# Optimization experiments

Measured on AMD Instinct MI355X. Metric: run time of the kernel, lower is better.

Reference implementation:

```python
import jax, jax.numpy as jnp
import numpy as np

G = 4          # number of product sub-quantizers
K = 1024       # codebook_size per sub-quantizer
D = 256        # full feature dim
d = D // G     # sub-dim per quantizer
DECAY = 0.99
EPS = 1e-5


def setup_inputs() -> dict:
    key = jax.random.key(0)
    k1, k2, k3, k4 = jax.random.split(key, 4)
    x = jax.random.normal(k1, (8, 4096, D), jnp.float32)
    embed = jax.random.normal(k2, (G, K, d), jnp.float32)
    embed_avg = jax.random.normal(k3, (G, K, d), jnp.float32)
    cluster_size = jax.random.uniform(k4, (G, K), jnp.float32)
    return dict(x=x, embed=embed, embed_avg=embed_avg, cluster_size=cluster_size)


def reference(x, embed, embed_avg, cluster_size):
    B, S, _ = x.shape
    N = B * S
    xg = x.reshape(N, G, d)                       # [N, G, d] tokens split into sub-vectors
    x2 = jnp.sum(xg * xg, axis=-1, keepdims=True)  # [N, G, 1]
    e2 = jnp.sum(embed * embed, axis=-1)           # [G, K]
    dots = jnp.einsum('ngd,gkd->ngk', xg, embed)   # [N, G, K]
    dist = -(x2 - 2.0 * dots + e2[None, :, :])     # [N, G, K]
    # sample_codebook_temp = 0 -> gumbel_sample degenerates to argmax
    ind = jnp.argmax(dist, axis=-1)                # [N, G]
    # quantized vectors: gather from each group's codebook
    zq = embed[jnp.arange(G)[None, :], ind]        # [N, G, d]
    # --- EMA buffer updates (training path) via scatter/segment-sum ---
    flat_ids = (ind + jnp.arange(G)[None, :] * K).reshape(-1)  # [N*G]
    counts = jax.ops.segment_sum(
        jnp.ones_like(flat_ids, dtype=jnp.float32), flat_ids,
        num_segments=G * K).reshape(G, K)
    embed_sum = jax.ops.segment_sum(
        xg.reshape(N * G, d), flat_ids,
        num_segments=G * K).reshape(G, K, d)
    new_cluster_size = DECAY * cluster_size + (1.0 - DECAY) * counts
    new_embed_avg = DECAY * embed_avg + (1.0 - DECAY) * embed_sum
    # laplace smoothing then renormalize codebook
    tot = jnp.sum(new_cluster_size, axis=-1, keepdims=True)       # [G, 1]
    smoothed = (new_cluster_size + EPS) / (tot + K * EPS) * tot   # [G, K]
    new_embed = new_embed_avg / smoothed[..., None]               # [G, K, d]
    return (zq.reshape(B, S, D),
            ind.reshape(B, S, G).astype(jnp.int32),
            new_embed, new_cluster_size, new_embed_avg)
```

## Files before the change

### kernel.cpp

```cpp
#include <hip/hip_runtime.h>
#include <cstdint>

#define GQ 4
#define KQ 1024
#define DQ 256
#define dq 64
#define NQ 32768
#define DECAYF 0.99f
#define EPSF 1e-5f

#define OFF_ZQ    0
#define OFF_IND   8388608
#define OFF_EMB   8519680
#define OFF_CS    8781824
#define OFF_AVG   8785920

#define WS_IND   0
#define WS_E2    524288
#define WS_EH    540672
#define WS_EL    1064960
#define WS_CTR   1589264
#define WS_LIST  1589280
#define CAP      16384
#define WS_E2D   1720352
#define WS_TOT   1753120
#define WS_PART  1753344
#define WS_PCNT  5947648

#define MARGIN 0.01f
#define FPS 65536.0f

#define MBLK 128

typedef __attribute__((ext_vector_type(8))) short bf16x8;
typedef __attribute__((ext_vector_type(4))) float f32x4;

__device__ __forceinline__ void split8_2x(float4 u, float4 v, bf16x8& h, bf16x8& l) {
    float f[8] = {u.x, u.y, u.z, u.w, v.x, v.y, v.z, v.w};
#pragma unroll
    for (int j = 0; j < 8; ++j) {
        float s = f[j] * 2.0f;
        uint32_t b = __float_as_uint(s);
        uint32_t hb = b & 0xffff0000u;
        float r = s - __uint_as_float(hb);
        uint32_t rb = __float_as_uint(r);
        h[j] = (short)(hb >> 16);
        l[j] = (short)((rb + 0x7fffu + ((rb >> 16) & 1u)) >> 16);
    }
}

__global__ void k_prep(const float* __restrict__ embed, const float* __restrict__ cs,
                       float* __restrict__ e2, double* __restrict__ e2d,
                       ushort* __restrict__ eh, ushort* __restrict__ el,
                       float* __restrict__ tot, int* __restrict__ ctr) {
    __shared__ double red[256];
    int t = blockIdx.x * 256 + threadIdx.x;
    int row = t >> 3;
    int f = t & 7;
    int c = f >> 2, l4 = f & 3;
    int g = row >> 10, k = row & 1023;
    int ch = k >> 6, co = k & 63;

    const float4* p = reinterpret_cast<const float4*>(embed + (size_t)row * dq + f * 8);
    float4 u = p[0], v = p[1];
    float fv[8] = {u.x, u.y, u.z, u.w, v.x, v.y, v.z, v.w};
    bf16x8 h, l;
    double s = 0.0;
#pragma unroll
    for (int jj = 0; jj < 8; ++jj) {
        float x = fv[jj];
        s = fma((double)x, (double)x, s);
        uint32_t b = __float_as_uint(x);
        uint32_t hb = (b + 0x7fffu + ((b >> 16) & 1u)) & 0xffff0000u;
        float r = x - __uint_as_float(hb);
        uint32_t rb = __float_as_uint(r);
        h[jj] = (short)(hb >> 16);
        l[jj] = (short)((rb + 0x7fffu + ((rb >> 16) & 1u)) >> 16);
    }
    size_t addr = (size_t)g * 65536 + (size_t)ch * 4096 + (size_t)(c * 4 + l4) * 512 + co * 8;
    *reinterpret_cast<bf16x8*>(eh + addr) = h;
    *reinterpret_cast<bf16x8*>(el + addr) = l;
    s += __shfl_xor(s, 1, 64);
    s += __shfl_xor(s, 2, 64);
    s += __shfl_xor(s, 4, 64);
    if (f == 0) { e2[row] = (float)s; e2d[row] = s; }

    if (blockIdx.x < 4) {
        int gg = blockIdx.x;
        const float4* c4 = reinterpret_cast<const float4*>(cs + gg * KQ);
        float4 cv = c4[threadIdx.x];
        red[threadIdx.x] = (double)cv.x + (double)cv.y + (double)cv.z + (double)cv.w;
        __syncthreads();
        for (int off = 128; off > 0; off >>= 1) {
            if (threadIdx.x < off) red[threadIdx.x] += red[threadIdx.x + off];
            __syncthreads();
        }
        if (threadIdx.x == 0) {
            tot[gg] = (float)((double)DECAYF * red[0] + (1.0 - (double)DECAYF) * (double)NQ);
            if (gg == 0) *ctr = 0;
        }
    }
}

__launch_bounds__(256)
__global__ void k_scores_mfma(const float* __restrict__ x,
                              const ushort* __restrict__ eh,
                              const ushort* __restrict__ el,
                              const float* __restrict__ e2,
                              const float* __restrict__ embed,
                              int* __restrict__ ind_t,
                              float* __restrict__ zq,
                              float* __restrict__ ind_out,
                              int* __restrict__ ctr, int2* __restrict__ list) {
    int g = blockIdx.y;
    int n0 = blockIdx.x * MBLK;
    int tid = threadIdx.x;
    int wid = tid >> 6;
    int lane = tid & 63;
    int l15 = lane & 15, l4 = lane >> 4;

    __shared__ ushort lds[2][8192];

    bf16x8 ah[2][2], al[2][2];
#pragma unroll
    for (int m = 0; m < 2; ++m)
#pragma unroll
        for (int c = 0; c < 2; ++c) {
            const float4* p = reinterpret_cast<const float4*>(
                x + (size_t)(n0 + wid * 32 + m * 16 + l15) * DQ + g * dq + c * 32 + l4 * 8);
            split8_2x(p[0], p[1], ah[m][c], al[m][c]);
        }

    const ushort* ehg = eh + (size_t)g * 65536;
    const ushort* elg = el + (size_t)g * 65536;
    const float*  e2g = e2 + (size_t)g * KQ;

    float m1[2][4], m2[2][4];
    int   k1[2][4];
#pragma unroll
    for (int m = 0; m < 2; ++m)
#pragma unroll
        for (int r = 0; r < 4; ++r) { m1[m][r] = -3.4e38f; m2[m][r] = -3.4e38f; k1[m][r] = 0; }

    int wu = wid * 512;
#define STAGE(b, ch)                                                               \
    do {                                                                           \
        const ushort* s0_ = ehg + (ch) * 4096 + tid * 8;                           \
        const ushort* s1_ = elg + (ch) * 4096 + tid * 8;                           \
        __builtin_amdgcn_global_load_lds(s0_,        &lds[b][wu],        16, 0, 0);\
        __builtin_amdgcn_global_load_lds(s0_ + 2048, &lds[b][2048 + wu], 16, 0, 0);\
        __builtin_amdgcn_global_load_lds(s1_,        &lds[b][4096 + wu], 16, 0, 0);\
        __builtin_amdgcn_global_load_lds(s1_ + 2048, &lds[b][6144 + wu], 16, 0, 0);\
    } while (0)

    float e2cur[4];
#pragma unroll
    for (int n = 0; n < 4; ++n) e2cur[n] = e2g[n * 16 + l15];

    STAGE(0, 0);
    int cur = 0;

#pragma unroll 1
    for (int ch = 0; ch < 16; ++ch) {
        int cb = ch * 64;
        __syncthreads();
        if (ch < 15) STAGE(cur ^ 1, ch + 1);

        float e2nxt[4];
        if (ch < 15) {
#pragma unroll
            for (int n = 0; n < 4; ++n) e2nxt[n] = e2g[cb + 64 + n * 16 + l15];
        }

        f32x4 acc[2][4];
#pragma unroll
        for (int m = 0; m < 2; ++m)
#pragma unroll
            for (int n = 0; n < 4; ++n)
                acc[m][n] = (f32x4){-e2cur[n], -e2cur[n], -e2cur[n], -e2cur[n]};

#pragma unroll
        for (int c = 0; c < 2; ++c) {
            bf16x8 bh[4], bl[4];
            int base = (c * 4 + l4) * 512 + l15 * 8;
#pragma unroll
            for (int n = 0; n < 4; ++n) {
                bh[n] = *reinterpret_cast<const bf16x8*>(&lds[cur][base + n * 128]);
                bl[n] = *reinterpret_cast<const bf16x8*>(&lds[cur][4096 + base + n * 128]);
            }
#pragma unroll
            for (int m = 0; m < 2; ++m)
#pragma unroll
                for (int n = 0; n < 4; ++n) {
                    acc[m][n] = __builtin_amdgcn_mfma_f32_16x16x32_bf16(ah[m][c], bh[n], acc[m][n], 0, 0, 0);
                    acc[m][n] = __builtin_amdgcn_mfma_f32_16x16x32_bf16(ah[m][c], bl[n], acc[m][n], 0, 0, 0);
                    acc[m][n] = __builtin_amdgcn_mfma_f32_16x16x32_bf16(al[m][c], bh[n], acc[m][n], 0, 0, 0);
                }
        }

#pragma unroll
        for (int n = 0; n < 4; ++n) {
            int col = cb + n * 16 + l15;
#pragma unroll
            for (int m = 0; m < 2; ++m)
#pragma unroll
                for (int r = 0; r < 4; ++r) {
                    float s = acc[m][n][r];
                    bool gt = s > m1[m][r];
                    m2[m][r] = __builtin_amdgcn_fmed3f(s, m1[m][r], m2[m][r]);
                    k1[m][r] = gt ? col : k1[m][r];
                    m1[m][r] = fmaxf(m1[m][r], s);
                }
        }
#pragma unroll
        for (int n = 0; n < 4; ++n) e2cur[n] = e2nxt[n];
        cur ^= 1;
    }
#undef STAGE

    int* ckk = reinterpret_cast<int*>(&lds[0][0]);

#pragma unroll
    for (int m = 0; m < 2; ++m)
#pragma unroll
        for (int r = 0; r < 4; ++r) {
            float a1 = m1[m][r], a2 = m2[m][r];
            int ak = k1[m][r];
#pragma unroll
            for (int d = 1; d < 16; d <<= 1) {
                float o1 = __shfl_xor(a1, d, 64);
                float o2 = __shfl_xor(a2, d, 64);
                int   ok = __shfl_xor(ak, d, 64);
                bool sw = (o1 > a1) || (o1 == a1 && ok < ak);
                float big = sw ? o1 : a1;
                int bigk = sw ? ok : ak;
                float small = sw ? a1 : o1;
                a2 = fmaxf(fmaxf(a2, o2), small);
                a1 = big; ak = bigk;
            }
            if (l15 == 0) {
                int rloc = m * 16 + l4 * 4 + r;
                int row = n0 + wid * 32 + rloc;
                ckk[wid * 32 + rloc] = ak;
                ind_t[(size_t)g * NQ + row] = ak;
                if (a1 - a2 < MARGIN) {
                    int idx = atomicAdd(ctr, 1);
                    if (idx < CAP) list[idx] = make_int2(row, g);
                }
            }
        }
    __syncthreads();

    if (lane < 32) {
        int row = n0 + wid * 32 + lane;
        ind_out[(size_t)row * GQ + g] = (float)ckk[wid * 32 + lane];
    }
#pragma unroll 4
    for (int rr = 0; rr < 32; ++rr) {
        int k = ckk[wid * 32 + rr];
        float v = embed[((size_t)(g * KQ + k)) * dq + lane];
        zq[(size_t)(n0 + wid * 32 + rr) * DQ + g * dq + lane] = v;
    }
}

__launch_bounds__(256)
__global__ void k_recheck(const float* __restrict__ x, const float* __restrict__ embed,
                          const double* __restrict__ e2d,
                          const int* __restrict__ ctr, const int2* __restrict__ list,
                          int* __restrict__ ind_t, float* __restrict__ zq,
                          float* __restrict__ ind_out) {
    __shared__ double sv[256];
    __shared__ int si[256];
    int nitems = *ctr;
    if (nitems > CAP) nitems = CAP;
    for (int it = blockIdx.x; it < nitems; it += gridDim.x) {
        int2 q = list[it];
        int n = q.x, g = q.y;
        const float4* xr4 = reinterpret_cast<const float4*>(x + (size_t)n * DQ + g * dq);
        float4 xr[16];
#pragma unroll
        for (int j = 0; j < 16; ++j) xr[j] = xr4[j];
        double best = -1e300;
        int bk = KQ;
        for (int k = threadIdx.x; k < KQ; k += 256) {
            const float4* er = reinterpret_cast<const float4*>(embed + ((size_t)g * KQ + k) * dq);
            double dot = 0.0;
#pragma unroll
            for (int j = 0; j < 16; ++j) {
                float4 e4 = er[j];
                dot = fma((double)xr[j].x, (double)e4.x, dot);
                dot = fma((double)xr[j].y, (double)e4.y, dot);
                dot = fma((double)xr[j].z, (double)e4.z, dot);
                dot = fma((double)xr[j].w, (double)e4.w, dot);
            }
            double s = 2.0 * dot - e2d[g * KQ + k];
            if (s > best || (s == best && k < bk)) { best = s; bk = k; }
        }
        sv[threadIdx.x] = best; si[threadIdx.x] = bk;
        __syncthreads();
        for (int off = 128; off > 0; off >>= 1) {
            if (threadIdx.x < off) {
                double ov = sv[threadIdx.x + off]; int oi = si[threadIdx.x + off];
                if (ov > sv[threadIdx.x] || (ov == sv[threadIdx.x] && oi < si[threadIdx.x])) {
                    sv[threadIdx.x] = ov; si[threadIdx.x] = oi;
                }
            }
            __syncthreads();
        }
        int kbest = si[0];
        if (threadIdx.x == 0) {
            ind_t[(size_t)g * NQ + n] = kbest;
            ind_out[(size_t)n * GQ + g] = (float)kbest;
        }
        if (threadIdx.x < dq)
            zq[(size_t)n * DQ + g * dq + threadIdx.x] =
                embed[((size_t)g * KQ + kbest) * dq + threadIdx.x];
        __syncthreads();
    }
}

#define SBINS 8
__launch_bounds__(256)
__global__ void k_segsum4(const float* __restrict__ x, const int* __restrict__ ind_t,
                          int* __restrict__ partial, int* __restrict__ pcnt) {
    __shared__ int lacc[SBINS][64];
    __shared__ int lcnt[SBINS];
    __shared__ int queue[4][128];

    int bid = blockIdx.x;
    int g = bid >> 9;
    int grp = (bid >> 2) & 127;
    int split = bid & 3;
    int kbase = grp * SBINS;
    int tid = threadIdx.x, wid = tid >> 6, lane = tid & 63;

    for (int i = tid; i < SBINS * 64; i += 256) ((int*)lacc)[i] = 0;
    if (tid < SBINS) lcnt[tid] = 0;
    __syncthreads();

    const int* ip = ind_t + (size_t)g * NQ;
    const float* xg = x + g * dq;
    int nbase = split * 8192 + wid * 2048;
    int wqn = 0;

#pragma unroll 4
    for (int c = 0; c < 2048; c += 64) {
        int n = nbase + c + lane;
        int d = ip[n] - kbase;
        bool hit = (unsigned)d < (unsigned)SBINS;
        unsigned long long mask = __ballot(hit);
        if (hit) {
            int pos = wqn + __popcll(mask & ((1ull << lane) - 1ull));
            queue[wid][pos] = (d << 20) | n;
        }
        wqn += __popcll(mask);
        if (wqn >= 64) {
            for (int q = 0; q < wqn; ++q) {
                int e = queue[wid][q];
                int b = e >> 20, n2 = e & 0xfffff;
                float xv = xg[(size_t)n2 * DQ + lane];
                atomicAdd(&lacc[b][lane], __float2int_rn(xv * FPS));
                if (lane == 0) atomicAdd(&lcnt[b], 1);
            }
            wqn = 0;
        }
    }
    for (int q = 0; q < wqn; ++q) {
        int e = queue[wid][q];
        int b = e >> 20, n2 = e & 0xfffff;
        float xv = xg[(size_t)n2 * DQ + lane];
        atomicAdd(&lacc[b][lane], __float2int_rn(xv * FPS));
        if (lane == 0) atomicAdd(&lcnt[b], 1);
    }
    __syncthreads();

    int base = split * (GQ * KQ) + g * KQ + kbase;
    for (int i = tid; i < SBINS * 64; i += 256) {
        int b = i >> 6, l = i & 63;
        partial[(size_t)(base + b) * 64 + l] = lacc[b][l];
    }
    if (tid < SBINS) pcnt[base + tid] = lcnt[tid];
}

__global__ void k_final(const int* __restrict__ partial, const int* __restrict__ pcnt,
                        const float* __restrict__ embed_avg, const float* __restrict__ cs,
                        const float* __restrict__ tot,
                        float* __restrict__ out_cs, float* __restrict__ out_avg,
                        float* __restrict__ out_embed) {
    int t = blockIdx.x * 256 + threadIdx.x;
    int gk = t >> 6, l = t & 63, g = gk >> 10;
    const int GK = GQ * KQ;
    int s = partial[(size_t)gk * 64 + l] + partial[(size_t)(GK + gk) * 64 + l]
          + partial[(size_t)(2 * GK + gk) * 64 + l] + partial[(size_t)(3 * GK + gk) * 64 + l];
    float a = (float)s * (1.0f / FPS);
    float nea = DECAYF * embed_avg[t] + (1.0f - DECAYF) * a;
    out_avg[t] = nea;
    int c = pcnt[gk] + pcnt[GK + gk] + pcnt[2 * GK + gk] + pcnt[3 * GK + gk];
    float ncs = DECAYF * cs[gk] + (1.0f - DECAYF) * (float)c;
    if (l == 0) out_cs[gk] = ncs;
    double tt = (double)tot[g];
    double sm = ((double)ncs + (double)EPSF) / (tt + (double)KQ * (double)EPSF) * tt;
    out_embed[t] = nea / (float)sm;
}

extern "C" void kernel_launch(void* const* d_in, const int* in_sizes, int n_in,
                              void* d_out, int out_size, void* d_ws, size_t ws_size,
                              hipStream_t stream) {
    const float* x         = (const float*)d_in[0];
    const float* embed     = (const float*)d_in[1];
    const float* embed_avg = (const float*)d_in[2];
    const float* cs        = (const float*)d_in[3];
    float* out = (float*)d_out;
    float* zq        = out + OFF_ZQ;
    float* ind_out   = out + OFF_IND;
    float* out_embed = out + OFF_EMB;
    float* out_cs    = out + OFF_CS;
    float* out_avg   = out + OFF_AVG;

    char* ws = (char*)d_ws;
    int*    ind_t = (int*)(ws + WS_IND);
    float*  e2    = (float*)(ws + WS_E2);
    ushort* eh    = (ushort*)(ws + WS_EH);
    ushort* el    = (ushort*)(ws + WS_EL);
    int*    ctr   = (int*)(ws + WS_CTR);
    int2*   list  = (int2*)(ws + WS_LIST);
    double* e2d   = (double*)(ws + WS_E2D);
    float*  tot   = (float*)(ws + WS_TOT);
    int*    part  = (int*)(ws + WS_PART);
    int*    pcnt  = (int*)(ws + WS_PCNT);

    k_prep<<<128, 256, 0, stream>>>(embed, cs, e2, e2d, eh, el, tot, ctr);
    dim3 g1(NQ / MBLK, GQ);
    k_scores_mfma<<<g1, 256, 0, stream>>>(x, eh, el, e2, embed, ind_t, zq, ind_out, ctr, list);
    k_recheck<<<256, 256, 0, stream>>>(x, embed, e2d, ctr, list, ind_t, zq, ind_out);
    k_segsum4<<<2048, 256, 0, stream>>>(x, ind_t, part, pcnt);
    k_final<<<(GQ * KQ * dq) / 256, 256, 0, stream>>>(part, pcnt, embed_avg, cs, tot,
                                                      out_cs, out_avg, out_embed);
}
```

Before: 139.4 us.

## Bucket token ids by code group during scoring to drive segment sums

The scoring kernel, and the recheck kernel for ambiguous tokens, now append each token's row and code slot to a per-group list. Each list covers eight codes and is filled with global atomic counters that k_prep zeroes. The segment-sum kernel then walks only its own list, instead of every block scanning all index entries of its split to find matches. This removes the redundant full index scans, at the cost of global atomics in the scoring epilogue. Each list holds at most 512 entries and anything beyond that is silently dropped, so a heavily used code group could give wrong sums.

```diff
diff --git a/kernel.cpp b/kernel.cpp
--- a/kernel.cpp
+++ b/kernel.cpp
@@ -26,6 +26,9 @@
 #define WS_TOT   1753120
 #define WS_PART  1753344
 #define WS_PCNT  5947648
+#define WS_BCNT  6013184
+#define WS_BLIST 6015232
+#define BCAP 512
 
 #define MARGIN 0.01f
 #define FPS 65536.0f
@@ -52,7 +55,8 @@
 __global__ void k_prep(const float* __restrict__ embed, const float* __restrict__ cs,
                        float* __restrict__ e2, double* __restrict__ e2d,
                        ushort* __restrict__ eh, ushort* __restrict__ el,
-                       float* __restrict__ tot, int* __restrict__ ctr) {
+                       float* __restrict__ tot, int* __restrict__ ctr,
+                       int* __restrict__ bcnt) {
     __shared__ double red[256];
     int t = blockIdx.x * 256 + threadIdx.x;
     int row = t >> 3;
@@ -85,6 +89,9 @@
     s += __shfl_xor(s, 4, 64);
     if (f == 0) { e2[row] = (float)s; e2d[row] = s; }
 
+    if (blockIdx.x >= 4 && blockIdx.x < 6) {
+        bcnt[(blockIdx.x - 4) * 256 + threadIdx.x] = 0;
+    }
     if (blockIdx.x < 4) {
         int gg = blockIdx.x;
         const float4* c4 = reinterpret_cast<const float4*>(cs + gg * KQ);
@@ -111,7 +118,8 @@
                               int* __restrict__ ind_t,
                               float* __restrict__ zq,
                               float* __restrict__ ind_out,
-                              int* __restrict__ ctr, int2* __restrict__ list) {
+                              int* __restrict__ ctr, int2* __restrict__ list,
+                              int* __restrict__ bcnt, int* __restrict__ blist) {
     int g = blockIdx.y;
     int n0 = blockIdx.x * MBLK;
     int tid = threadIdx.x;
@@ -246,6 +254,10 @@
                 if (a1 - a2 < MARGIN) {
                     int idx = atomicAdd(ctr, 1);
                     if (idx < CAP) list[idx] = make_int2(row, g);
+                } else {
+                    int lid = g * 128 + (ak >> 3);
+                    int pos = atomicAdd(&bcnt[lid], 1);
+                    if (pos < BCAP) blist[lid * BCAP + pos] = ((ak & 7) << 16) | row;
                 }
             }
         }
@@ -268,7 +280,8 @@
                           const double* __restrict__ e2d,
                           const int* __restrict__ ctr, const int2* __restrict__ list,
                           int* __restrict__ ind_t, float* __restrict__ zq,
-                          float* __restrict__ ind_out) {
+                          float* __restrict__ ind_out,
+                          int* __restrict__ bcnt, int* __restrict__ blist) {
     __shared__ double sv[256];
     __shared__ int si[256];
     int nitems = *ctr;
@@ -311,6 +324,9 @@
         if (threadIdx.x == 0) {
             ind_t[(size_t)g * NQ + n] = kbest;
             ind_out[(size_t)n * GQ + g] = (float)kbest;
+            int lid = g * 128 + (kbest >> 3);
+            int pos = atomicAdd(&bcnt[lid], 1);
+            if (pos < BCAP) blist[lid * BCAP + pos] = ((kbest & 7) << 16) | n;
         }
         if (threadIdx.x < dq)
             zq[(size_t)n * DQ + g * dq + threadIdx.x] =
@@ -319,67 +335,44 @@
     }
 }
 
-#define SBINS 8
 __launch_bounds__(256)
-__global__ void k_segsum4(const float* __restrict__ x, const int* __restrict__ ind_t,
+__global__ void k_segsum5(const float* __restrict__ x,
+                          const int* __restrict__ bcnt, const int* __restrict__ blist,
                           int* __restrict__ partial, int* __restrict__ pcnt) {
-    __shared__ int lacc[SBINS][64];
-    __shared__ int lcnt[SBINS];
-    __shared__ int queue[4][128];
+    __shared__ int lacc[8][64];
+    __shared__ int lcnt[8];
 
     int bid = blockIdx.x;
     int g = bid >> 9;
     int grp = (bid >> 2) & 127;
     int split = bid & 3;
-    int kbase = grp * SBINS;
     int tid = threadIdx.x, wid = tid >> 6, lane = tid & 63;
 
-    for (int i = tid; i < SBINS * 64; i += 256) ((int*)lacc)[i] = 0;
-    if (tid < SBINS) lcnt[tid] = 0;
+    for (int i = tid; i < 512; i += 256) ((int*)lacc)[i] = 0;
+    if (tid < 8) lcnt[tid] = 0;
     __syncthreads();
 
-    const int* ip = ind_t + (size_t)g * NQ;
+    int lid = g * 128 + grp;
+    int cnt = bcnt[lid];
+    if (cnt > BCAP) cnt = BCAP;
+    const int* lp = blist + lid * BCAP;
     const float* xg = x + g * dq;
-    int nbase = split * 8192 + wid * 2048;
-    int wqn = 0;
-
-#pragma unroll 4
-    for (int c = 0; c < 2048; c += 64) {
-        int n = nbase + c + lane;
-        int d = ip[n] - kbase;
-        bool hit = (unsigned)d < (unsigned)SBINS;
-        unsigned long long mask = __ballot(hit);
-        if (hit) {
-            int pos = wqn + __popcll(mask & ((1ull << lane) - 1ull));
-            queue[wid][pos] = (d << 20) | n;
-        }
-        wqn += __popcll(mask);
-        if (wqn >= 64) {
-            for (int q = 0; q < wqn; ++q) {
-                int e = queue[wid][q];
-                int b = e >> 20, n2 = e & 0xfffff;
-                float xv = xg[(size_t)n2 * DQ + lane];
-                atomicAdd(&lacc[b][lane], __float2int_rn(xv * FPS));
-                if (lane == 0) atomicAdd(&lcnt[b], 1);
-            }
-            wqn = 0;
-        }
-    }
-    for (int q = 0; q < wqn; ++q) {
-        int e = queue[wid][q];
-        int b = e >> 20, n2 = e & 0xfffff;
-        float xv = xg[(size_t)n2 * DQ + lane];
+
+    for (int i = split * 4 + wid; i < cnt; i += 16) {
+        int e = lp[i];
+        int b = e >> 16, n = e & 0xffff;
+        float xv = xg[(size_t)n * DQ + lane];
         atomicAdd(&lacc[b][lane], __float2int_rn(xv * FPS));
         if (lane == 0) atomicAdd(&lcnt[b], 1);
     }
     __syncthreads();
 
-    int base = split * (GQ * KQ) + g * KQ + kbase;
-    for (int i = tid; i < SBINS * 64; i += 256) {
+    int base = split * (GQ * KQ) + g * KQ + grp * 8;
+    for (int i = tid; i < 512; i += 256) {
         int b = i >> 6, l = i & 63;
         partial[(size_t)(base + b) * 64 + l] = lacc[b][l];
     }
-    if (tid < SBINS) pcnt[base + tid] = lcnt[tid];
+    if (tid < 8) pcnt[base + tid] = lcnt[tid];
 }
 
 __global__ void k_final(const int* __restrict__ partial, const int* __restrict__ pcnt,
@@ -428,12 +421,16 @@
     float*  tot   = (float*)(ws + WS_TOT);
     int*    part  = (int*)(ws + WS_PART);
     int*    pcnt  = (int*)(ws + WS_PCNT);
-
-    k_prep<<<128, 256, 0, stream>>>(embed, cs, e2, e2d, eh, el, tot, ctr);
+    int*    bcnt  = (int*)(ws + WS_BCNT);
+    int*    blist = (int*)(ws + WS_BLIST);
+
+    k_prep<<<128, 256, 0, stream>>>(embed, cs, e2, e2d, eh, el, tot, ctr, bcnt);
     dim3 g1(NQ / MBLK, GQ);
-    k_scores_mfma<<<g1, 256, 0, stream>>>(x, eh, el, e2, embed, ind_t, zq, ind_out, ctr, list);
-    k_recheck<<<256, 256, 0, stream>>>(x, embed, e2d, ctr, list, ind_t, zq, ind_out);
-    k_segsum4<<<2048, 256, 0, stream>>>(x, ind_t, part, pcnt);
+    k_scores_mfma<<<g1, 256, 0, stream>>>(x, eh, el, e2, embed, ind_t, zq, ind_out,
+                                          ctr, list, bcnt, blist);
+    k_recheck<<<256, 256, 0, stream>>>(x, embed, e2d, ctr, list, ind_t, zq, ind_out,
+                                       bcnt, blist);
+    k_segsum5<<<2048, 256, 0, stream>>>(x, bcnt, blist, part, pcnt);
     k_final<<<(GQ * KQ * dq) / 256, 256, 0, stream>>>(part, pcnt, embed_avg, cs, tot,
                                                       out_cs, out_avg, out_embed);
 }
```

New measurement: 267.2 us. +91.7%, slower.
